# Kernel optimization log

Measured on AMD Instinct MI355X. Metric: run time of the kernel, lower is better.

The kernel has to match this reference:

```python
import jax, jax.numpy as jnp
import numpy as np

NUM_EMBEDDINGS = 2048
EMBEDDING_DIM = 256
COMMITMENT_COST = 0.25


def setup_inputs() -> dict:
    key = jax.random.key(0)
    k1, k2 = jax.random.split(key)
    inputs = jax.random.normal(k1, (2, EMBEDDING_DIM, 24, 24, 24), dtype=jnp.float32)
    embedding_weight = jax.random.normal(k2, (NUM_EMBEDDINGS, EMBEDDING_DIM), dtype=jnp.float32)
    return {"inputs": inputs, "embedding_weight": embedding_weight}


def reference(inputs, embedding_weight):
    # [B, C, D, H, W] -> [B, D, H, W, C]
    x = jnp.transpose(inputs, (0, 2, 3, 4, 1))
    in_shape = x.shape
    flat = x.reshape(-1, EMBEDDING_DIM)  # [N, D]

    distances = (
        jnp.sum(flat * flat, axis=1, keepdims=True)
        + jnp.sum(embedding_weight * embedding_weight, axis=1)
        - 2.0 * flat @ embedding_weight.T
    )
    encoding_indices = jnp.argmin(distances, axis=1)  # [N]
    encodings = jax.nn.one_hot(encoding_indices, NUM_EMBEDDINGS, dtype=jnp.float32)  # [N, K]

    # Gather instead of one_hot @ W (same math, no redundant GEMM)
    quantized = embedding_weight[encoding_indices].reshape(in_shape)

    e_latent_loss = jnp.mean((jax.lax.stop_gradient(quantized) - x) ** 2)
    loss = COMMITMENT_COST * e_latent_loss

    # Straight-through estimator
    quantized_st = x + jax.lax.stop_gradient(quantized - x)

    avg_probs = jnp.mean(encodings, axis=0)
    perplexity = jnp.exp(-jnp.sum(avg_probs * jnp.log(avg_probs + 1e-10)))

    quantized_out = jnp.transpose(quantized_st, (0, 4, 1, 2, 3))
    return (loss, quantized_out, perplexity, encodings, encoding_indices[:, None])
```

## Files before the change

### kernel.cpp

```cpp
#include <hip/hip_runtime.h>

#define S_SP   13824
#define CHAN   256
#define NQ     27648
#define KCODES 2048
#define CS     3538944
#define OFF_Q   1
#define OFF_PPL 7077889
#define OFF_ENC 7077890LL
#define OFF_IDX 63700994LL
#define DIST_BLKS 432

typedef __bf16 bf16x8 __attribute__((ext_vector_type(8)));
typedef float  f32x4  __attribute__((ext_vector_type(4)));

#define GLOAD_LDS16(g, s)                                                      \
  __builtin_amdgcn_global_load_lds(                                            \
      (const __attribute__((address_space(1))) void*)(g),                      \
      (__attribute__((address_space(3))) void*)(s), 16, 0, 0)

__device__ __forceinline__ unsigned int f2bf(float f) {
  unsigned int u = __float_as_uint(f);
  unsigned int r = u + 0x7FFFu + ((u >> 16) & 1u);
  return r >> 16;
}
__device__ __forceinline__ float bf2f(unsigned int h) {
  return __uint_as_float(h << 16);
}
__device__ __forceinline__ void fsplit(float f, unsigned int& hi, unsigned int& lo) {
  hi = f2bf(f);
  float r = f - bf2f(hi);
  lo = f2bf(r);
}

__global__ __launch_bounds__(256) void prep_wx(const float* __restrict__ W,
                                               const float* __restrict__ X,
                                               unsigned short* __restrict__ Wh,
                                               unsigned short* __restrict__ Wl,
                                               float* __restrict__ wn,
                                               unsigned short* __restrict__ Xh,
                                               unsigned short* __restrict__ Xl,
                                               float* __restrict__ xn,
                                               int* __restrict__ zero_base) {
  __shared__ float xs[32 * 257];
  int t = threadIdx.x;
  if (blockIdx.x < 256) {
    if (blockIdx.x == 0) {
      for (int j = t; j < 2050; j += 256) zero_base[j] = 0;
    }
    int g = blockIdx.x * 256 + t;
    int row = g >> 5;
    int d0 = (g & 31) * 8;
    const float* Wp = W + (size_t)row * CHAN + d0;
    float v[8];
    *(float4*)(v) = *(const float4*)Wp;
    *(float4*)(v + 4) = *(const float4*)(Wp + 4);
    float s = 0.f;
    unsigned int h[8], l[8];
#pragma unroll
    for (int j = 0; j < 8; ++j) {
      s = fmaf(v[j], v[j], s);
      fsplit(v[j], h[j], l[j]);
    }
    int4 ph, pl;
    ph.x = (int)(h[0] | (h[1] << 16)); ph.y = (int)(h[2] | (h[3] << 16));
    ph.z = (int)(h[4] | (h[5] << 16)); ph.w = (int)(h[6] | (h[7] << 16));
    pl.x = (int)(l[0] | (l[1] << 16)); pl.y = (int)(l[2] | (l[3] << 16));
    pl.z = (int)(l[4] | (l[5] << 16)); pl.w = (int)(l[6] | (l[7] << 16));
    *(int4*)(Wh + (size_t)row * CHAN + d0) = ph;
    *(int4*)(Wl + (size_t)row * CHAN + d0) = pl;
    for (int off = 16; off; off >>= 1) s += __shfl_down(s, off);
    if ((t & 31) == 0) wn[row] = s;
    return;
  }
  int qb = (blockIdx.x - 256) * 32;
  int b = qb / S_SP, s0 = qb % S_SP;
  const float* xp = X + (size_t)b * CS + s0;
  int q = t & 31;
  int db = t >> 5;
  for (int r = 0; r < 32; ++r) {
    int d = db + (r << 3);
    xs[q * 257 + d] = xp[(size_t)d * S_SP + q];
  }
  __syncthreads();
  int row = t >> 3, c8 = t & 7;
  size_t obase = (size_t)(qb + row) * CHAN;
  const float* rp0 = xs + row * 257;
  float ss = 0.f;
#pragma unroll
  for (int j = 0; j < 4; ++j) {
    int d = j * 64 + c8 * 8;
    const float* rp = rp0 + d;
    unsigned int h[8], l[8];
#pragma unroll
    for (int e = 0; e < 8; ++e) {
      float v = rp[e];
      ss = fmaf(v, v, ss);
      fsplit(v, h[e], l[e]);
    }
    int4 ph, pl;
    ph.x = (int)(h[0] | (h[1] << 16)); ph.y = (int)(h[2] | (h[3] << 16));
    ph.z = (int)(h[4] | (h[5] << 16)); ph.w = (int)(h[6] | (h[7] << 16));
    pl.x = (int)(l[0] | (l[1] << 16)); pl.y = (int)(l[2] | (l[3] << 16));
    pl.z = (int)(l[4] | (l[5] << 16)); pl.w = (int)(l[6] | (l[7] << 16));
    *(int4*)(Xh + obase + d) = ph;
    *(int4*)(Xl + obase + d) = pl;
  }
  ss += __shfl_xor(ss, 1);
  ss += __shfl_xor(ss, 2);
  ss += __shfl_xor(ss, 4);
  if (c8 == 0) xn[qb + row] = ss;
}

__global__ __launch_bounds__(256, 2) void dist_mfma(const unsigned short* __restrict__ Xh,
                                                    const unsigned short* __restrict__ Xl,
                                                    const unsigned short* __restrict__ Wh,
                                                    const unsigned short* __restrict__ Wl,
                                                    const float* __restrict__ wn,
                                                    float* __restrict__ rB1,
                                                    int* __restrict__ rI1,
                                                    float* __restrict__ rB2,
                                                    float* __restrict__ outF) {
  __shared__ __align__(16) unsigned short sW[2][2][4096];
  __shared__ float wnl[1024];
  int t = threadIdx.x;

  if (blockIdx.x >= DIST_BLKS) {
    int bid2 = blockIdx.x - DIST_BLKS;
    f32x4 z = {0.f, 0.f, 0.f, 0.f};
    float* rp = outF + OFF_ENC + (size_t)bid2 * 16 * KCODES + t * 4;
#pragma unroll 4
    for (int q = 0; q < 16; ++q) {
      *(f32x4*)rp = z;
      *(f32x4*)(rp + 1024) = z;
      rp += KCODES;
    }
    return;
  }

  int w = t >> 6, l = t & 63;
  int lr = l & 15, lc = l >> 4;
  int kg = blockIdx.x & 1;
  int qb = (blockIdx.x >> 1) * 128;
  int kofs = kg << 10;

  for (int j = t; j < 1024; j += 256) wnl[j] = wn[kofs + j];

  bf16x8 ah[2][8], al[2][8];
#pragma unroll
  for (int s = 0; s < 2; ++s) {
    size_t base = (size_t)(qb + w * 32 + s * 16 + lr) * CHAN + lc * 8;
#pragma unroll
    for (int c = 0; c < 8; ++c) {
      ah[s][c] = *(const bf16x8*)(Xh + base + c * 32);
      al[s][c] = *(const bf16x8*)(Xl + base + c * 32);
    }
  }

  float b1[2][4], b2[2][4]; int i1[2][4];
#pragma unroll
  for (int s = 0; s < 2; ++s)
#pragma unroll
    for (int r = 0; r < 4; ++r) { b1[s][r] = 3.4e38f; b2[s][r] = 3.4e38f; i1[s][r] = 0; }

  auto stage = [&](int buf, int kt) {
    size_t rb = (size_t)(kofs + (kt << 4) + lr) * CHAN + lc * 8;
    GLOAD_LDS16(Wh + rb + w * 32,        &sW[buf][0][w * 512]);
    GLOAD_LDS16(Wh + rb + (w + 4) * 32,  &sW[buf][0][(w + 4) * 512]);
    GLOAD_LDS16(Wl + rb + w * 32,        &sW[buf][1][w * 512]);
    GLOAD_LDS16(Wl + rb + (w + 4) * 32,  &sW[buf][1][(w + 4) * 512]);
  };

  auto compute = [&](int cur, f32x4& o0, f32x4& o1) {
    f32x4 a0 = {0.f, 0.f, 0.f, 0.f}, a1 = {0.f, 0.f, 0.f, 0.f};
#pragma unroll
    for (int c = 0; c < 8; ++c) {
      bf16x8 bh = *(const bf16x8*)&sW[cur][0][c * 512 + (l << 3)];
      bf16x8 bl = *(const bf16x8*)&sW[cur][1][c * 512 + (l << 3)];
      a0 = __builtin_amdgcn_mfma_f32_16x16x32_bf16(ah[0][c], bh, a0, 0, 0, 0);
      a1 = __builtin_amdgcn_mfma_f32_16x16x32_bf16(ah[1][c], bh, a1, 0, 0, 0);
      a0 = __builtin_amdgcn_mfma_f32_16x16x32_bf16(al[0][c], bh, a0, 0, 0, 0);
      a1 = __builtin_amdgcn_mfma_f32_16x16x32_bf16(al[1][c], bh, a1, 0, 0, 0);
      a0 = __builtin_amdgcn_mfma_f32_16x16x32_bf16(ah[0][c], bl, a0, 0, 0, 0);
      a1 = __builtin_amdgcn_mfma_f32_16x16x32_bf16(ah[1][c], bl, a1, 0, 0, 0);
    }
    o0 = a0; o1 = a1;
  };

  auto select = [&](const f32x4& a0, const f32x4& a1, int k, float wnk) {
#pragma unroll
    for (int r = 0; r < 4; ++r) {
      float s0 = fmaf(-2.0f, a0[r], wnk);
      bool lt0 = s0 < b1[0][r];
      b2[0][r] = fminf(b2[0][r], fmaxf(s0, b1[0][r]));
      b1[0][r] = lt0 ? s0 : b1[0][r];
      i1[0][r] = lt0 ? k : i1[0][r];
      float s1 = fmaf(-2.0f, a1[r], wnk);
      bool lt1 = s1 < b1[1][r];
      b2[1][r] = fminf(b2[1][r], fmaxf(s1, b1[1][r]));
      b1[1][r] = lt1 ? s1 : b1[1][r];
      i1[1][r] = lt1 ? k : i1[1][r];
    }
  };

  stage(0, 0);
  __syncthreads();

  f32x4 pa0, pa1;
  int   pk   = kofs + lr;
  float pwnk = wnl[lr];
  stage(1, 1);
  compute(0, pa0, pa1);
  __syncthreads();

  for (int kt = 1; kt < 64; ++kt) {
    int cur = kt & 1;
    if (kt < 63) stage(cur ^ 1, kt + 1);
    f32x4 a0, a1;
    compute(cur, a0, a1);
    select(pa0, pa1, pk, pwnk);
    pa0 = a0; pa1 = a1;
    pk = kofs + (kt << 4) + lr;
    pwnk = wnl[(kt << 4) + lr];
    __syncthreads();
  }
  select(pa0, pa1, pk, pwnk);

#pragma unroll
  for (int m = 1; m < 16; m <<= 1) {
#pragma unroll
    for (int s = 0; s < 2; ++s)
#pragma unroll
      for (int r = 0; r < 4; ++r) {
        float ob1 = __shfl_xor(b1[s][r], m);
        int   oi  = __shfl_xor(i1[s][r], m);
        float ob2 = __shfl_xor(b2[s][r], m);
        bool sw = (ob1 < b1[s][r]) || (ob1 == b1[s][r] && oi < i1[s][r]);
        b2[s][r] = fminf(fmaxf(b1[s][r], ob1), fminf(b2[s][r], ob2));
        b1[s][r] = sw ? ob1 : b1[s][r];
        i1[s][r] = sw ? oi : i1[s][r];
      }
  }
  if (lr == 0) {
#pragma unroll
    for (int s = 0; s < 2; ++s)
#pragma unroll
      for (int r = 0; r < 4; ++r) {
        int q = qb + w * 32 + s * 16 + lc * 4 + r;
        size_t o = (size_t)kg * NQ + q;
        rB1[o] = b1[s][r]; rI1[o] = i1[s][r]; rB2[o] = b2[s][r];
      }
  }
}

__global__ __launch_bounds__(256) void merge_k(const float* __restrict__ rB1,
                                               const int* __restrict__ rI1,
                                               const float* __restrict__ rB2,
                                               const float* __restrict__ xn,
                                               float* __restrict__ idx_out,
                                               int* __restrict__ flagcount,
                                               int2* __restrict__ flaglist,
                                               int* __restrict__ counts,
                                               float* __restrict__ loss_acc) {
  __shared__ float wred[4];
  int t = threadIdx.x;
  int n = blockIdx.x * 256 + t;
  float B1 = rB1[n]; int I1 = rI1[n]; float B2 = rB2[n];
  float c1 = rB1[NQ + n]; int ci = rI1[NQ + n]; float c2 = rB2[NQ + n];
  bool sw = (c1 < B1) || (c1 == B1 && ci < I1);
  float nb2 = fminf(fmaxf(B1, c1), fminf(B2, c2));
  float nb1 = sw ? c1 : B1;
  int   ni  = sw ? ci : I1;
  if (nb2 - nb1 < 0.05f) {
    int slot = atomicAdd(flagcount, 1);
    flaglist[slot] = make_int2(n, ni);
  }
  idx_out[n] = (float)ni;
  atomicAdd(&counts[ni], 1);

  float lq = xn[n] + nb1;
  for (int off = 32; off; off >>= 1) lq += __shfl_down(lq, off);
  if ((t & 63) == 0) wred[t >> 6] = lq;
  __syncthreads();
  if (t == 0) atomicAdd(loss_acc, wred[0] + wred[1] + wred[2] + wred[3]);
}

__global__ __launch_bounds__(256) void refine2(const float* __restrict__ X,
                                               const float* __restrict__ W,
                                               const int* __restrict__ flagcount,
                                               const int2* __restrict__ flaglist,
                                               float* __restrict__ idx_out,
                                               int* __restrict__ counts) {
  __shared__ double xd[CHAN];
  __shared__ double rv[256];
  __shared__ int    ri[256];
  int t = threadIdx.x;
  int cnt = flagcount[0];
  for (int jj = blockIdx.x; jj < cnt; jj += gridDim.x) {
    __syncthreads();
    int2 e = flaglist[jj];
    int n = e.x, prov = e.y;
    int b = n / S_SP, s = n % S_SP;
    xd[t] = (double)X[(size_t)b * CS + (size_t)t * S_SP + s];
    __syncthreads();

    double best = 1e300;
    int bi = 1 << 30;
    for (int j8 = 0; j8 < 8; ++j8) {
      int k = t * 8 + j8;
      const float* Wp = W + (size_t)k * CHAN;
      double dsum = 0.0;
      for (int d = 0; d < CHAN; ++d) {
        double df = xd[d] - (double)Wp[d];
        dsum = fma(df, df, dsum);
      }
      if (dsum < best) { best = dsum; bi = k; }
    }
    rv[t] = best; ri[t] = bi;
    __syncthreads();
    for (int off = 128; off > 0; off >>= 1) {
      if (t < off) {
        if (rv[t + off] < rv[t] || (rv[t + off] == rv[t] && ri[t + off] < ri[t])) {
          rv[t] = rv[t + off]; ri[t] = ri[t + off];
        }
      }
      __syncthreads();
    }
    if (t == 0) {
      int fin = ri[0];
      idx_out[n] = (float)fin;
      if (fin != prov) {
        atomicAdd(&counts[prov], -1);
        atomicAdd(&counts[fin], 1);
      }
    }
  }
}

__global__ __launch_bounds__(256) void emit_og(const float* __restrict__ W,
                                               float* __restrict__ outF) {
  __shared__ int sidx[64];
  int t = threadIdx.x;
  int qb = blockIdx.x * 64;
  if (t < 64) sidx[t] = (int)outF[OFF_IDX + qb + t];
  __syncthreads();
  if (t < 64) outF[OFF_ENC + (size_t)(qb + t) * KCODES + sidx[t]] = 1.0f;

  int q = t & 63, cg = t >> 6;
  int n = qb + q;
  int idx = sidx[q];
  int b = n / S_SP, s = n % S_SP;
  const float* Wp = W + (size_t)idx * CHAN;
  float* qp = outF + OFF_Q + (size_t)b * CS + s;
#pragma unroll 8
  for (int k = 0; k < 64; ++k) {
    int c = cg + (k << 2);
    qp[(size_t)c * S_SP] = Wp[c];
  }
}

__global__ __launch_bounds__(256) void finalize(const int* __restrict__ counts,
                                                const float* __restrict__ loss_acc,
                                                float* __restrict__ outF) {
  __shared__ double red[256];
  int t = threadIdx.x;
  double H = 0.0;
  for (int k = t; k < KCODES; k += 256) {
    double p = (double)counts[k] / (double)NQ;
    H += p * log(p + 1e-10);
  }
  red[t] = H;
  __syncthreads();
  for (int off = 128; off > 0; off >>= 1) {
    if (t < off) red[t] += red[t + off];
    __syncthreads();
  }
  if (t == 0) {
    outF[0] = 0.25f * (loss_acc[0] / 7077888.0f);
    outF[OFF_PPL] = (float)exp(-red[0]);
  }
}

extern "C" void kernel_launch(void* const* d_in, const int* in_sizes, int n_in,
                              void* d_out, int out_size, void* d_ws, size_t ws_size,
                              hipStream_t stream) {
  const float* X = (const float*)d_in[0];
  const float* W = (const float*)d_in[1];
  float* outF = (float*)d_out;
  char* ws = (char*)d_ws;
  float* wn        = (float*)ws;
  int*   counts    = (int*)(ws + 8192);
  float* loss_acc  = (float*)(ws + 16384);
  int*   flagcount = (int*)(ws + 16388);
  int2*  flaglist  = (int2*)(ws + 32768);
  float* rB1       = (float*)(ws + 262144);
  int*   rI1       = (int*)(ws + 483328);
  float* rB2       = (float*)(ws + 704512);
  float* xn        = (float*)(ws + 925696);
  unsigned short* Wh = (unsigned short*)(ws + 1048576);
  unsigned short* Wl = (unsigned short*)(ws + 2097152);
  unsigned short* Xh = (unsigned short*)(ws + 3145728);
  unsigned short* Xl = Xh + (size_t)NQ * CHAN;

  prep_wx<<<256 + NQ / 32, 256, 0, stream>>>(W, X, Wh, Wl, wn, Xh, Xl, xn,
                                             (int*)(ws + 8192));
  dist_mfma<<<DIST_BLKS + NQ / 16, 256, 0, stream>>>(Xh, Xl, Wh, Wl, wn,
                                                     rB1, rI1, rB2, outF);
  merge_k<<<NQ / 256, 256, 0, stream>>>(rB1, rI1, rB2, xn, outF + OFF_IDX,
                                        flagcount, flaglist, counts, loss_acc);
  refine2<<<256, 256, 0, stream>>>(X, W, flagcount, flaglist, outF + OFF_IDX, counts);
  emit_og<<<NQ / 64, 256, 0, stream>>>(W, outF);
  finalize<<<1, 256, 0, stream>>>(counts, loss_acc, outF);
}
```

Measured before the change: 222.6 us.

## Fuse merge with output emission and patch refined rows afterward

Merges the top-2 candidate merge kernel with the one-hot and quantized-output emission kernel, so outputs are written straight from the provisional argmin without re-reading the index buffer. The refinement kernel now runs last and patches only the rows whose index changed: it fixes the one-hot row, the counts and the quantized column. This removes one launch and a global round trip of indices. In exchange the loss reduction now runs on only 64 lanes per block, with more atomics, and refined rows are written twice.

```diff
diff --git a/kernel.cpp b/kernel.cpp
--- a/kernel.cpp
+++ b/kernel.cpp
@@ -253,44 +253,62 @@
   }
 }
 
-__global__ __launch_bounds__(256) void merge_k(const float* __restrict__ rB1,
-                                               const int* __restrict__ rI1,
-                                               const float* __restrict__ rB2,
-                                               const float* __restrict__ xn,
-                                               float* __restrict__ idx_out,
-                                               int* __restrict__ flagcount,
-                                               int2* __restrict__ flaglist,
-                                               int* __restrict__ counts,
-                                               float* __restrict__ loss_acc) {
-  __shared__ float wred[4];
+__global__ __launch_bounds__(256) void emit_all(const float* __restrict__ rB1,
+                                                const int* __restrict__ rI1,
+                                                const float* __restrict__ rB2,
+                                                const float* __restrict__ xn,
+                                                const float* __restrict__ W,
+                                                float* __restrict__ outF,
+                                                int* __restrict__ flagcount,
+                                                int2* __restrict__ flaglist,
+                                                int* __restrict__ counts,
+                                                float* __restrict__ loss_acc) {
+  __shared__ int sidx[64];
   int t = threadIdx.x;
-  int n = blockIdx.x * 256 + t;
-  float B1 = rB1[n]; int I1 = rI1[n]; float B2 = rB2[n];
-  float c1 = rB1[NQ + n]; int ci = rI1[NQ + n]; float c2 = rB2[NQ + n];
-  bool sw = (c1 < B1) || (c1 == B1 && ci < I1);
-  float nb2 = fminf(fmaxf(B1, c1), fminf(B2, c2));
-  float nb1 = sw ? c1 : B1;
-  int   ni  = sw ? ci : I1;
-  if (nb2 - nb1 < 0.05f) {
-    int slot = atomicAdd(flagcount, 1);
-    flaglist[slot] = make_int2(n, ni);
-  }
-  idx_out[n] = (float)ni;
-  atomicAdd(&counts[ni], 1);
-
-  float lq = xn[n] + nb1;
-  for (int off = 32; off; off >>= 1) lq += __shfl_down(lq, off);
-  if ((t & 63) == 0) wred[t >> 6] = lq;
+  int qb = blockIdx.x * 64;
+
+  if (t < 64) {
+    int n = qb + t;
+    float B1 = rB1[n]; int I1 = rI1[n]; float B2 = rB2[n];
+    float c1 = rB1[NQ + n]; int ci = rI1[NQ + n]; float c2 = rB2[NQ + n];
+    bool sw = (c1 < B1) || (c1 == B1 && ci < I1);
+    float nb2 = fminf(fmaxf(B1, c1), fminf(B2, c2));
+    float nb1 = sw ? c1 : B1;
+    int   ni  = sw ? ci : I1;
+    if (nb2 - nb1 < 0.05f) {
+      int slot = atomicAdd(flagcount, 1);
+      flaglist[slot] = make_int2(n, ni);
+    }
+    sidx[t] = ni;
+    outF[OFF_IDX + n] = (float)ni;
+    atomicAdd(&counts[ni], 1);
+    outF[OFF_ENC + (size_t)n * KCODES + ni] = 1.0f;
+
+    float lq = xn[n] + nb1;
+    for (int off = 32; off; off >>= 1) lq += __shfl_down(lq, off);
+    if (t == 0) atomicAdd(loss_acc, lq);
+  }
   __syncthreads();
-  if (t == 0) atomicAdd(loss_acc, wred[0] + wred[1] + wred[2] + wred[3]);
-}
-
-__global__ __launch_bounds__(256) void refine2(const float* __restrict__ X,
-                                               const float* __restrict__ W,
-                                               const int* __restrict__ flagcount,
-                                               const int2* __restrict__ flaglist,
-                                               float* __restrict__ idx_out,
-                                               int* __restrict__ counts) {
+
+  int q = t & 63, cg = t >> 6;
+  int n = qb + q;
+  int idx = sidx[q];
+  int b = n / S_SP, s = n % S_SP;
+  const float* Wp = W + (size_t)idx * CHAN;
+  float* qp = outF + OFF_Q + (size_t)b * CS + s;
+#pragma unroll 8
+  for (int k = 0; k < 64; ++k) {
+    int c = cg + (k << 2);
+    qp[(size_t)c * S_SP] = Wp[c];
+  }
+}
+
+__global__ __launch_bounds__(256) void refine_patch(const float* __restrict__ X,
+                                                    const float* __restrict__ W,
+                                                    const int* __restrict__ flagcount,
+                                                    const int2* __restrict__ flaglist,
+                                                    float* __restrict__ outF,
+                                                    int* __restrict__ counts) {
   __shared__ double xd[CHAN];
   __shared__ double rv[256];
   __shared__ int    ri[256];
@@ -326,36 +344,20 @@
       }
       __syncthreads();
     }
-    if (t == 0) {
-      int fin = ri[0];
-      idx_out[n] = (float)fin;
-      if (fin != prov) {
+    int fin = ri[0];
+    __syncthreads();
+    if (fin != prov) {
+      if (t == 0) {
+        outF[OFF_IDX + n] = (float)fin;
         atomicAdd(&counts[prov], -1);
         atomicAdd(&counts[fin], 1);
+        float* row = outF + OFF_ENC + (size_t)n * KCODES;
+        row[prov] = 0.0f;
+        row[fin]  = 1.0f;
       }
-    }
-  }
-}
-
-__global__ __launch_bounds__(256) void emit_og(const float* __restrict__ W,
-                                               float* __restrict__ outF) {
-  __shared__ int sidx[64];
-  int t = threadIdx.x;
-  int qb = blockIdx.x * 64;
-  if (t < 64) sidx[t] = (int)outF[OFF_IDX + qb + t];
-  __syncthreads();
-  if (t < 64) outF[OFF_ENC + (size_t)(qb + t) * KCODES + sidx[t]] = 1.0f;
-
-  int q = t & 63, cg = t >> 6;
-  int n = qb + q;
-  int idx = sidx[q];
-  int b = n / S_SP, s = n % S_SP;
-  const float* Wp = W + (size_t)idx * CHAN;
-  float* qp = outF + OFF_Q + (size_t)b * CS + s;
-#pragma unroll 8
-  for (int k = 0; k < 64; ++k) {
-    int c = cg + (k << 2);
-    qp[(size_t)c * S_SP] = Wp[c];
+      float* qp = outF + OFF_Q + (size_t)b * CS + s;
+      qp[(size_t)t * S_SP] = W[(size_t)fin * CHAN + t];
+    }
   }
 }
 
@@ -406,9 +408,8 @@
                                              (int*)(ws + 8192));
   dist_mfma<<<DIST_BLKS + NQ / 16, 256, 0, stream>>>(Xh, Xl, Wh, Wl, wn,
                                                      rB1, rI1, rB2, outF);
-  merge_k<<<NQ / 256, 256, 0, stream>>>(rB1, rI1, rB2, xn, outF + OFF_IDX,
+  emit_all<<<NQ / 64, 256, 0, stream>>>(rB1, rI1, rB2, xn, W, outF,
                                         flagcount, flaglist, counts, loss_acc);
-  refine2<<<256, 256, 0, stream>>>(X, W, flagcount, flaglist, outF + OFF_IDX, counts);
-  emit_og<<<NQ / 64, 256, 0, stream>>>(W, outF);
+  refine_patch<<<256, 256, 0, stream>>>(X, W, flagcount, flaglist, outF, counts);
   finalize<<<1, 256, 0, stream>>>(counts, loss_acc, outF);
 }
```

Measured after the change: 219.4 us. No clear change (-1.4%).
